# Kernel tuning notes

Measured on AMD Instinct MI355X. Metric: run time of the kernel, lower is better.

## Reference

```python
import math
import jax, jax.numpy as jnp
import numpy as np

WS = 4            # window size
LS = 2 * WS       # local context size
NH = 8            # num heads
DIM = 128
EPS = 1e-5


def setup_inputs() -> dict:
    key = jax.random.key(0)
    ks = jax.random.split(key, 8)
    B, C, H, W = 4, DIM, 48, 48
    features = jax.random.normal(ks[0], (B, C, H, W), dtype=jnp.float32)
    s = 0.02
    return {
        'features': features,
        'ln_w': jnp.ones((C,), jnp.float32),
        'ln_b': jnp.zeros((C,), jnp.float32),
        'q_w': jax.random.normal(ks[1], (C, C), jnp.float32) * s,
        'q_b': jnp.zeros((C,), jnp.float32),
        'kv_w': jax.random.normal(ks[2], (2 * C, C), jnp.float32) * s,
        'kv_b': jnp.zeros((2 * C,), jnp.float32),
        'out_w': jax.random.normal(ks[3], (C, C), jnp.float32) * s,
        'out_b': jnp.zeros((C,), jnp.float32),
    }


def _avgpool_tokens(x, k):
    # x: [B,C,H,W] -> [B, (H//k)*(W//k), C]
    B, C, H, W = x.shape
    t = x.reshape(B, C, H // k, k, W // k, k).mean(axis=(3, 5))
    return t.reshape(B, C, -1).transpose(0, 2, 1)


def reference(features, ln_w, ln_b, q_w, q_b, kv_w, kv_b, out_w, out_b):
    B, C, H, W = features.shape
    Hw, Ww = H // WS, W // WS
    nw = Hw * Ww
    hd = C // NH

    # ---- window partition: [B,C,H,W] -> [B*nw, WS*WS, C]
    qt = features.reshape(B, C, Hw, WS, Ww, WS).transpose(0, 2, 4, 3, 5, 1)
    qt = qt.reshape(B * nw, WS * WS, C)

    # ---- LayerNorm(dim)
    mu = qt.mean(-1, keepdims=True)
    var = qt.var(-1, keepdims=True)
    qt = (qt - mu) / jnp.sqrt(var + EPS) * ln_w + ln_b

    # ---- local context: pad to target, unfold kernel=LS stride=WS
    target = (int(math.sqrt(nw)) - 1) * WS + LS
    ph, pw = max(0, target - H), max(0, target - W)
    pad = ((0, 0), (0, 0), (ph // 2, ph - ph // 2), (pw // 2, pw - pw // 2))
    padded = jnp.pad(features, pad)
    # channel order of patches is (C, kh, kw), same as torch unfold
    patches = jax.lax.conv_general_dilated_patches(
        padded, filter_shape=(LS, LS), window_strides=(WS, WS), padding='VALID')
    local = patches.reshape(B, C, LS * LS, nw).transpose(0, 3, 2, 1)
    local = local.reshape(B * nw, LS * LS, C)

    # ---- multi-scale pooled tokens, broadcast to each window
    mid = _avgpool_tokens(features, 2)      # [B, M, C]
    glo = _avgpool_tokens(features, 4)      # [B, G, C]
    mid = jnp.broadcast_to(mid[:, None], (B, nw) + mid.shape[1:]).reshape(B * nw, -1, C)
    glo = jnp.broadcast_to(glo[:, None], (B, nw) + glo.shape[1:]).reshape(B * nw, -1, C)

    kv_tokens = jnp.concatenate([local, mid, glo], axis=1)  # [B*nw, Nkv, C]

    # ---- projections (torch Linear: x @ W.T + b)
    queries = qt @ q_w.T + q_b
    kv = kv_tokens @ kv_w.T + kv_b
    keys, values = kv[..., :C], kv[..., C:]

    # ---- multi-head attention
    Nq, Nkv = queries.shape[1], keys.shape[1]
    q = queries.reshape(-1, Nq, NH, hd)
    k = keys.reshape(-1, Nkv, NH, hd)
    v = values.reshape(-1, Nkv, NH, hd)
    scores = jnp.einsum('bqhd,bkhd->bhqk', q, k) / math.sqrt(hd)
    weights = jax.nn.softmax(scores, axis=-1)
    attended = jnp.einsum('bhqk,bkhd->bqhd', weights, v).reshape(-1, Nq, C)

    out = attended @ out_w.T + out_b

    # ---- window reconstruction -> [B,C,H,W]
    out = out.reshape(B, Hw, Ww, WS, WS, C).transpose(0, 5, 1, 3, 2, 4)
    out = out.reshape(B, C, H, W)
    return out + features
```

## Files before the change

### kernel.cpp

```cpp
#include <hip/hip_runtime.h>


typedef unsigned short u16;
typedef short v8s __attribute__((ext_vector_type(8)));
typedef v8s __attribute__((may_alias)) v8s_am;
typedef short v4s __attribute__((ext_vector_type(4)));
typedef v4s __attribute__((may_alias)) v4s_am;
typedef float v4f __attribute__((ext_vector_type(4)));

#define MFMA_BF16(a, b, c) __builtin_amdgcn_mfma_f32_16x16x32_bf16(a, b, c, 0, 0, 0)

#if __has_builtin(__builtin_amdgcn_mfma_f32_16x16x16bf16_1k)
#define MFMA16(a, b, c) __builtin_amdgcn_mfma_f32_16x16x16bf16_1k(a, b, c, 0, 0, 0)
#else
static __device__ __forceinline__ v4f mfma16_fb(v4s a, v4s b, v4f c) {
    v8s a8 = {a[0], a[1], a[2], a[3], 0, 0, 0, 0};
    v8s b8 = {b[0], b[1], b[2], b[3], 0, 0, 0, 0};
    return MFMA_BF16(a8, b8, c);
}
#define MFMA16(a, b, c) mfma16_fb(a, b, c)
#endif

#if __has_builtin(__builtin_amdgcn_exp2f)
#define EXP2(x) __builtin_amdgcn_exp2f(x)
#else
#define EXP2(x) exp2f(x)
#endif

__device__ __forceinline__ float b2f(u16 u) {
    union { unsigned int i; float f; } x;
    x.i = ((unsigned int)u) << 16;
    return x.f;
}
__device__ __forceinline__ u16 f2b(float f) {
    union { float f; unsigned int i; } x;
    x.f = f;
    unsigned int u = x.i;
    return (u16)((u + 0x7fffu + ((u >> 16) & 1u)) >> 16);
}

__global__ __launch_bounds__(256) void k_transpose_prep(
    const float* __restrict__ F,
    const float* __restrict__ qw, const float* __restrict__ kvw,
    const float* __restrict__ ow,
    const float* __restrict__ lnw, const float* __restrict__ lnb,
    u16* __restrict__ Xt, u16* __restrict__ Wb, float* __restrict__ MuRs)
{
    int blk = blockIdx.x;
    int t = threadIdx.x;
    if (blk >= 288) {
        int base = (blk - 288) * 4096 + t * 16;
#pragma unroll
        for (int i = 0; i < 4; ++i) {
            int idx = base + i * 4;
            const float* src; int off;
            if (idx < 16384)      { src = qw;  off = idx; }
            else if (idx < 49152) { src = kvw; off = idx - 16384; }
            else                  { src = ow;  off = idx - 49152; }
            float4 v = *(const float4*)(src + off);
            unsigned long long packed =
                (unsigned long long)f2b(v.x) |
                ((unsigned long long)f2b(v.y) << 16) |
                ((unsigned long long)f2b(v.z) << 32) |
                ((unsigned long long)f2b(v.w) << 48);
            *(unsigned long long*)(Wb + idx) = packed;
        }
        if (blk == 288) {
            Wb[65536 + t] = f2b(t < 128 ? lnw[t] : lnb[t - 128]);
        }
        return;
    }
    __shared__ u16 X[128][34];
    int b = blk / 72;
    int p0 = (blk % 72) * 32;
#pragma unroll 4
    for (int i = 0; i < 16; ++i) {
        int c = i * 8 + (t >> 5);
        int pix = t & 31;
        X[c][pix] = f2b(F[((size_t)(b * 128 + c)) * 2304 + p0 + pix]);
    }
    __syncthreads();
    int pix = t >> 3;
    int c0 = (t & 7) * 16;
    size_t row = (size_t)(b * 2304 + p0 + pix) * 128;
    float s = 0.f, s2 = 0.f;
#pragma unroll
    for (int sg = 0; sg < 2; ++sg) {
        v8s raw;
#pragma unroll
        for (int j = 0; j < 8; ++j) {
            u16 u = X[c0 + sg * 8 + j][pix];
            raw[j] = (short)u;
            float v = b2f(u);
            s += v; s2 += v * v;
        }
        *(v8s_am*)&Xt[row + c0 + sg * 8] = raw;
    }
    s += __shfl_xor(s, 1);  s2 += __shfl_xor(s2, 1);
    s += __shfl_xor(s, 2);  s2 += __shfl_xor(s2, 2);
    s += __shfl_xor(s, 4);  s2 += __shfl_xor(s2, 4);
    if ((t & 7) == 0) {
        float mean = s * (1.f / 128.f);
        float var = s2 * (1.f / 128.f) - mean * mean;
        float rstd = rsqrtf(var + 1e-5f);
        MuRs[(b * 2304 + p0 + pix) * 2]     = mean;
        MuRs[(b * 2304 + p0 + pix) * 2 + 1] = rstd;
    }
}

__global__ __launch_bounds__(256) void k_pool(
    const float* __restrict__ F, u16* __restrict__ Pml)
{
    int gid = blockIdx.x * 256 + threadIdx.x;
    int row = gid >> 4;
    int seg = gid & 15;
    v8s outv;
    if (row < 2304) {
        int b = row / 576, r = row % 576;
        int i = r / 24, j = r % 24;
#pragma unroll
        for (int jc = 0; jc < 8; ++jc) {
            int c = seg * 8 + jc;
            const float* src = F + ((size_t)(b * 128 + c)) * 2304 + (2 * i) * 48 + 2 * j;
            float2 a = *(const float2*)src;
            float2 d = *(const float2*)(src + 48);
            outv[jc] = (short)f2b((a.x + a.y + d.x + d.y) * 0.25f);
        }
    } else {
        int r2 = row - 2304;
        int b = r2 / 144, r = r2 % 144;
        int i = r / 12, j = r % 12;
#pragma unroll
        for (int jc = 0; jc < 8; ++jc) {
            int c = seg * 8 + jc;
            const float* src = F + ((size_t)(b * 128 + c)) * 2304 + (4 * i) * 48 + 4 * j;
            float s = 0.f;
#pragma unroll
            for (int di = 0; di < 4; ++di) {
                float4 v = *(const float4*)(src + di * 48);
                s += (v.x + v.y) + (v.z + v.w);
            }
            outv[jc] = (short)f2b(s * 0.0625f);
        }
    }
    *(v8s_am*)&Pml[((size_t)row) * 128 + seg * 8] = outv;
}

__global__ __launch_bounds__(256) void k_gemm_kv(
    const u16* __restrict__ Pml,
    const u16* __restrict__ W,
    const float* __restrict__ bias,
    u16* __restrict__ KVg,
    u16* __restrict__ VTg)
{
    __shared__ u16 Al[64][136];
    __shared__ u16 Wl[64][136];
    int tm = blockIdx.x * 64, tn = blockIdx.y * 64;
    int t = threadIdx.x;
    {
        int seg = t & 15, r0 = t >> 4;
#pragma unroll
        for (int i = 0; i < 4; ++i) {
            int r = r0 + 16 * i;
            *(v8s_am*)&Al[r][seg * 8] = *(const v8s_am*)&Pml[((size_t)(tm + r)) * 128 + seg * 8];
            *(v8s_am*)&Wl[r][seg * 8] = *(const v8s_am*)&W[((size_t)(tn + r)) * 128 + seg * 8];
        }
    }
    __syncthreads();
    int lane = t & 63, wave = t >> 6;
    int n15 = lane & 15, quad = lane >> 4;
    int wm = (wave & 1) * 32, wn = (wave >> 1) * 32;
    v4f acc[2][2] = {};
#pragma unroll
    for (int kc = 0; kc < 4; ++kc) {
        v8s a[2], bb[2];
#pragma unroll
        for (int im = 0; im < 2; ++im)
            a[im] = *(const v8s_am*)&Al[wm + im * 16 + n15][kc * 32 + quad * 8];
#pragma unroll
        for (int in = 0; in < 2; ++in)
            bb[in] = *(const v8s_am*)&Wl[wn + in * 16 + n15][kc * 32 + quad * 8];
#pragma unroll
        for (int im = 0; im < 2; ++im)
#pragma unroll
            for (int in = 0; in < 2; ++in)
                acc[im][in] = MFMA_BF16(a[im], bb[in], acc[im][in]);
    }
#pragma unroll
    for (int in = 0; in < 2; ++in) {
        int n = tn + wn + in * 16 + n15;
        float bv = bias[n];
#pragma unroll
        for (int im = 0; im < 2; ++im) {
            int mbase = tm + wm + im * 16 + quad * 4;
#pragma unroll
            for (int r = 0; r < 4; ++r) {
                int m = mbase + r;
                u16 h = f2b(acc[im][in][r] + bv);
                if (n < 128) {
                    KVg[((size_t)m) * 128 + n] = h;
                } else {
                    int ch = n - 128, bb2, tok;
                    if (m < 2304) { bb2 = m / 576; tok = m % 576; }
                    else { int r2 = m - 2304; bb2 = r2 / 144; tok = 576 + r2 % 144; }
                    VTg[((size_t)(bb2 * 128 + ch)) * 720 + tok] = h;
                }
            }
        }
    }
}

__global__ __launch_bounds__(256, 3) void k_attn_fused(
    const float* __restrict__ F,
    const u16* __restrict__ Xt,
    const float* __restrict__ MuRs,
    const u16* __restrict__ KVg,
    const u16* __restrict__ VTg,
    const u16* __restrict__ Wb,
    const float* __restrict__ qb,
    const float* __restrict__ kvb,
    const float* __restrict__ ob,
    float* __restrict__ Out)
{
    __shared__ u16 KB[2][64][136];
    __shared__ u16 VtAt[4][32][68];

    const u16* qwb  = Wb;
    const u16* kvwb = Wb + 16384;
    const u16* owb  = Wb + 49152;
    const u16* lnwb = Wb + 65536;
    const u16* lnbb = Wb + 65664;
    u16* At = &VtAt[0][0][0];

    int w = blockIdx.x;
    int b = w / 144, wr = (w % 144) / 12, wc = w % 12;
    int t = threadIdx.x;
    int lane = t & 63, wave = t >> 6, n15 = lane & 15, quad = lane >> 4;
    v8s zf8 = {};
    v4f zz4 = {0.f, 0.f, 0.f, 0.f};
    const float QSCALE = 0.25f * 1.44269504f;

    v8s stg[4];
#pragma unroll
    for (int i = 0; i < 4; ++i) {
        int chunk = t * 4 + i;
        stg[i] = *(const v8s_am*)&KVg[((size_t)(b * 576 + (chunk >> 4))) * 128 + (chunk & 15) * 8];
    }

    int qh = wr * 4 + (n15 >> 2), qw_ = wc * 4 + (n15 & 3);
    int qpix = b * 2304 + qh * 48 + qw_;
    float mu = MuRs[qpix * 2], rstd = MuRs[qpix * 2 + 1];
    v8s xln[4];
#pragma unroll
    for (int kc = 0; kc < 4; ++kc) {
        v8s x  = *(const v8s_am*)&Xt[(size_t)qpix * 128 + kc * 32 + quad * 8];
        v8s lw = *(const v8s_am*)&lnwb[kc * 32 + quad * 8];
        v8s lb = *(const v8s_am*)&lnbb[kc * 32 + quad * 8];
        v8s y;
#pragma unroll
        for (int j = 0; j < 8; ++j)
            y[j] = (short)f2b((b2f((u16)x[j]) - mu) * rstd * b2f((u16)lw[j]) + b2f((u16)lb[j]));
        xln[kc] = y;
    }

    v4s qf2[2];
#pragma unroll
    for (int e = 0; e < 2; ++e) {
        int n0 = wave * 16 + e * 64;
        v4f qacc = zz4;
#pragma unroll
        for (int kc = 0; kc < 4; ++kc) {
            v8s aw = *(const v8s_am*)&qwb[((size_t)(n0 + n15)) * 128 + kc * 32 + quad * 8];
            qacc = MFMA_BF16(aw, xln[kc], qacc);
        }
        v4s q4;
#pragma unroll
        for (int r = 0; r < 4; ++r)
            q4[r] = (short)f2b((qacc[r] + qb[n0 + quad * 4 + r]) * QSCALE);
        qf2[e] = q4;
    }

    v4s kfloc[2][4];
#pragma unroll
    for (int g = 0; g < 4; ++g) {
        int tl = g * 16 + n15;
        int fh = tl >> 3, fw = tl & 7;
        int hh = wr * 4 - 2 + fh, ww = wc * 4 - 2 + fw;
        bool valid = (hh >= 0 && hh < 48 && ww >= 0 && ww < 48);
        size_t arow = (size_t)(b * 2304 + hh * 48 + ww) * 128;
        v8s xb[4];
#pragma unroll
        for (int kc = 0; kc < 4; ++kc) {
            v8s v = zf8;
            if (valid) v = *(const v8s_am*)&Xt[arow + kc * 32 + quad * 8];
            xb[kc] = v;
        }
#pragma unroll
        for (int s = 0; s < 4; ++s) {
            int sbase = (s & 1) * 64 + (s >> 1) * 128 + wave * 16;
            v4f acc = zz4;
#pragma unroll
            for (int kc = 0; kc < 4; ++kc) {
                v8s aw = *(const v8s_am*)&kvwb[((size_t)(sbase + n15)) * 128 + kc * 32 + quad * 8];
                acc = MFMA_BF16(aw, xb[kc], acc);
            }
            if (s < 2) {
                v4s k4;
#pragma unroll
                for (int r = 0; r < 4; ++r)
                    k4[r] = (short)f2b(acc[r] + kvb[sbase + quad * 4 + r]);
                kfloc[s][g] = k4;
            } else {
                int e = s - 2;
#pragma unroll
                for (int r = 0; r < 4; ++r)
                    VtAt[wave][e * 16 + quad * 4 + r][g * 16 + n15] =
                        f2b(acc[r] + kvb[sbase + quad * 4 + r]);
            }
        }
    }

    v4f oacc[2] = {};
    float ls[2] = {0.f, 0.f};
    const u16* VTb = VTg + (size_t)b * 128 * 720;

    asm volatile("s_waitcnt lgkmcnt(0)" ::: "memory");
#pragma unroll
    for (int g = 0; g < 4; ++g) {
#pragma unroll
        for (int e = 0; e < 2; ++e) {
            v4f St = MFMA16(kfloc[e][g], qf2[e], zz4);
            float p0 = EXP2(St[0]), p1 = EXP2(St[1]);
            float p2 = EXP2(St[2]), p3 = EXP2(St[3]);
            ls[e] += (p0 + p1) + (p2 + p3);
            v4s pk = {(short)f2b(p0), (short)f2b(p1), (short)f2b(p2), (short)f2b(p3)};
            v4s vf = *(const v4s_am*)&VtAt[wave][e * 16 + n15][g * 16 + quad * 4];
            oacc[e] = MFMA16(vf, pk, oacc[e]);
        }
    }

#pragma unroll
    for (int i = 0; i < 4; ++i) {
        int chunk = t * 4 + i;
        *(v8s_am*)&KB[1][chunk >> 4][(chunk & 15) * 8] = stg[i];
    }
    __syncthreads();

    for (int tb = 0; tb <= 10; ++tb) {
        v4s vp[2][4];
#pragma unroll
        for (int e = 0; e < 2; ++e) {
            int head = wave + e * 4;
            const u16* vrow = VTb + (size_t)(head * 16 + n15) * 720 + tb * 64 + quad * 4;
#pragma unroll
            for (int g = 0; g < 4; ++g)
                vp[e][g] = *(const v4s_am*)(vrow + g * 16);
        }
        int nt_ = tb + 1;
        int rowbase = (nt_ < 9) ? (b * 576 + nt_ * 64)
                                : (2304 + b * 144 + nt_ * 64 - 576);
        int nrows = (nt_ == 11) ? 16 : 64;
        bool sv[4];
#pragma unroll
        for (int i = 0; i < 4; ++i) {
            int chunk = t * 4 + i;
            int rr = chunk >> 4;
            sv[i] = rr < nrows;
            if (sv[i])
                stg[i] = *(const v8s_am*)&KVg[((size_t)(rowbase + rr)) * 128 + (chunk & 15) * 8];
        }
        const u16 (*KBc)[136] = KB[1 - (tb & 1)];
#pragma unroll
        for (int g = 0; g < 4; ++g) {
#pragma unroll
            for (int e = 0; e < 2; ++e) {
                int head = wave + e * 4;
                v4s kf = *(const v4s_am*)&KBc[g * 16 + n15][head * 16 + quad * 4];
                v4f St = MFMA16(kf, qf2[e], zz4);
                float p0 = EXP2(St[0]), p1 = EXP2(St[1]);
                float p2 = EXP2(St[2]), p3 = EXP2(St[3]);
                ls[e] += (p0 + p1) + (p2 + p3);
                v4s pk = {(short)f2b(p0), (short)f2b(p1), (short)f2b(p2), (short)f2b(p3)};
                oacc[e] = MFMA16(vp[e][g], pk, oacc[e]);
            }
        }
#pragma unroll
        for (int i = 0; i < 4; ++i) {
            if (sv[i]) {
                int chunk = t * 4 + i;
                *(v8s_am*)&KB[tb & 1][chunk >> 4][(chunk & 15) * 8] = stg[i];
            }
        }
        __syncthreads();
    }
#pragma unroll
    for (int e = 0; e < 2; ++e) {
        int head = wave + e * 4;
        v4s vf = *(const v4s_am*)(VTb + (size_t)(head * 16 + n15) * 720 + 704 + quad * 4);
        v4s kf = *(const v4s_am*)&KB[0][n15][head * 16 + quad * 4];
        v4f St = MFMA16(kf, qf2[e], zz4);
        float p0 = EXP2(St[0]), p1 = EXP2(St[1]);
        float p2 = EXP2(St[2]), p3 = EXP2(St[3]);
        ls[e] += (p0 + p1) + (p2 + p3);
        v4s pk = {(short)f2b(p0), (short)f2b(p1), (short)f2b(p2), (short)f2b(p3)};
        oacc[e] = MFMA16(vf, pk, oacc[e]);
    }

#pragma unroll
    for (int e = 0; e < 2; ++e) {
        ls[e] += __shfl_xor(ls[e], 16);
        ls[e] += __shfl_xor(ls[e], 32);
        float inv = 1.f / ls[e];
        int head = wave + e * 4;
        v4s a4 = {(short)f2b(oacc[e][0] * inv), (short)f2b(oacc[e][1] * inv),
                  (short)f2b(oacc[e][2] * inv), (short)f2b(oacc[e][3] * inv)};
        *(v4s_am*)&At[n15 * 136 + head * 16 + quad * 4] = a4;
    }
    __syncthreads();

    {
        int n0 = wave * 32;
        v4f oa[2] = {};
#pragma unroll
        for (int kc = 0; kc < 4; ++kc) {
            v8s af = *(const v8s_am*)&At[n15 * 136 + kc * 32 + quad * 8];
#pragma unroll
            for (int in = 0; in < 2; ++in) {
                v8s bf = *(const v8s_am*)&owb[((size_t)(n0 + in * 16 + n15)) * 128 + kc * 32 + quad * 8];
                oa[in] = MFMA_BF16(af, bf, oa[in]);
            }
        }
#pragma unroll
        for (int in = 0; in < 2; ++in) {
            int c = n0 + in * 16 + n15;
            float bv = ob[c];
#pragma unroll
            for (int r = 0; r < 4; ++r) {
                int pix = quad * 4 + r;
                int hh = wr * 4 + (pix >> 2), ww_ = wc * 4 + (pix & 3);
                size_t idx = ((size_t)(b * 128 + c)) * 2304 + hh * 48 + ww_;
                Out[idx] = oa[in][r] + bv + F[idx];
            }
        }
    }
}

extern "C" void kernel_launch(void* const* d_in, const int* in_sizes, int n_in,
                              void* d_out, int out_size, void* d_ws, size_t ws_size,
                              hipStream_t stream)
{
    const float* F   = (const float*)d_in[0];
    const float* lnw = (const float*)d_in[1];
    const float* lnb = (const float*)d_in[2];
    const float* qw  = (const float*)d_in[3];
    const float* qb  = (const float*)d_in[4];
    const float* kvw = (const float*)d_in[5];
    const float* kvb = (const float*)d_in[6];
    const float* ow  = (const float*)d_in[7];
    const float* ob  = (const float*)d_in[8];
    float* Out = (float*)d_out;

    u16* ws    = (u16*)d_ws;
    u16* Xt    = ws;
    u16* Pml   = Xt + 9216 * 128;
    u16* KVg   = Pml + 2880 * 128;
    u16* VTg   = KVg + 2880 * 128;
    u16* Wb    = VTg + 4 * 128 * 720;
    float* MuRs = (float*)(Wb + 65792);
    u16* kvwb = Wb + 16384;

    k_transpose_prep<<<304, 256, 0, stream>>>(F, qw, kvw, ow, lnw, lnb, Xt, Wb, MuRs);
    k_pool<<<180, 256, 0, stream>>>(F, Pml);
    k_gemm_kv<<<dim3(45, 4), 256, 0, stream>>>(Pml, kvwb, kvb, KVg, VTg);
    k_attn_fused<<<576, 256, 0, stream>>>(F, Xt, MuRs, KVg, VTg, Wb,
                                          qb, kvb, ob, Out);
}
```

Before: 137.2 us.

## Load K/V fragments directly to registers with double buffering, drop LDS staging

The attention loop no longer stages the shared K tile through LDS with per-tile __syncthreads. Each wave now loads its K and V fragments straight from global memory into registers, ping-ponging between two register fragment sets so the next tile's loads overlap the current tile's MFMA and exp work. The smaller LDS footprint lets the launch bound rise to 4 blocks per CU, and block indices are remapped so each XCD handles windows of a single batch image for L2 locality. In exchange, register pressure goes up and global/L2 traffic increases, since K is no longer shared across waves through LDS.

```diff
diff --git a/kernel.cpp b/kernel.cpp
--- a/kernel.cpp
+++ b/kernel.cpp
@@ -210,7 +210,54 @@
     }
 }
 
-__global__ __launch_bounds__(256, 3) void k_attn_fused(
+struct Frag { v4s k[2][4]; v4s v[2][4]; };
+
+__device__ __forceinline__ void load_tile(Frag& f, const u16* kb0, const u16* vb0,
+                                          int rb128, int t64)
+{
+#pragma unroll
+    for (int e = 0; e < 2; ++e)
+#pragma unroll
+        for (int g = 0; g < 4; ++g) {
+            f.k[e][g] = *(const v4s_am*)(kb0 + e * 64 + rb128 + g * 2048);
+            f.v[e][g] = *(const v4s_am*)(vb0 + e * 46080 + t64 + g * 16);
+        }
+}
+
+__device__ __forceinline__ void load_tile11(Frag& f, const u16* kb0, const u16* vb0,
+                                            int b)
+{
+    int rb128 = 294912 + b * 18432 + 16384;
+#pragma unroll
+    for (int e = 0; e < 2; ++e) {
+        f.k[e][0] = *(const v4s_am*)(kb0 + e * 64 + rb128);
+        f.v[e][0] = *(const v4s_am*)(vb0 + e * 46080 + 704);
+    }
+}
+
+__device__ __forceinline__ int rb128f(int b, int t) {
+    return (t < 9) ? (b * 73728 + t * 8192) : (294912 + b * 18432 + (t - 9) * 8192);
+}
+
+template<int NG>
+__device__ __forceinline__ void tile_attn(const Frag& f, const v4s* qf2,
+                                          v4f* oacc, float* ls)
+{
+    v4f zz = {0.f, 0.f, 0.f, 0.f};
+#pragma unroll
+    for (int g = 0; g < NG; ++g)
+#pragma unroll
+        for (int e = 0; e < 2; ++e) {
+            v4f St = MFMA16(f.k[e][g], qf2[e], zz);
+            float p0 = EXP2(St[0]), p1 = EXP2(St[1]);
+            float p2 = EXP2(St[2]), p3 = EXP2(St[3]);
+            ls[e] += (p0 + p1) + (p2 + p3);
+            v4s pk = {(short)f2b(p0), (short)f2b(p1), (short)f2b(p2), (short)f2b(p3)};
+            oacc[e] = MFMA16(f.v[e][g], pk, oacc[e]);
+        }
+}
+
+__global__ __launch_bounds__(256, 4) void k_attn_fused(
     const float* __restrict__ F,
     const u16* __restrict__ Xt,
     const float* __restrict__ MuRs,
@@ -222,30 +269,26 @@
     const float* __restrict__ ob,
     float* __restrict__ Out)
 {
-    __shared__ u16 KB[2][64][136];
-    __shared__ u16 VtAt[4][32][68];
+    __shared__ u16 VtW[4][32][68];
+    __shared__ u16 At[16][136];
 
     const u16* qwb  = Wb;
     const u16* kvwb = Wb + 16384;
     const u16* owb  = Wb + 49152;
     const u16* lnwb = Wb + 65536;
     const u16* lnbb = Wb + 65664;
-    u16* At = &VtAt[0][0][0];
-
-    int w = blockIdx.x;
-    int b = w / 144, wr = (w % 144) / 12, wc = w % 12;
+
+    int blk = blockIdx.x;
+    int xcd = blk & 7, jj = blk >> 3;
+    int b = xcd >> 1;
+    int wr = (xcd & 1) * 6 + jj / 12;
+    int wc = jj % 12;
+
     int t = threadIdx.x;
     int lane = t & 63, wave = t >> 6, n15 = lane & 15, quad = lane >> 4;
     v8s zf8 = {};
     v4f zz4 = {0.f, 0.f, 0.f, 0.f};
     const float QSCALE = 0.25f * 1.44269504f;
-
-    v8s stg[4];
-#pragma unroll
-    for (int i = 0; i < 4; ++i) {
-        int chunk = t * 4 + i;
-        stg[i] = *(const v8s_am*)&KVg[((size_t)(b * 576 + (chunk >> 4))) * 128 + (chunk & 15) * 8];
-    }
 
     int qh = wr * 4 + (n15 >> 2), qw_ = wc * 4 + (n15 & 3);
     int qpix = b * 2304 + qh * 48 + qw_;
@@ -314,15 +357,19 @@
                 int e = s - 2;
 #pragma unroll
                 for (int r = 0; r < 4; ++r)
-                    VtAt[wave][e * 16 + quad * 4 + r][g * 16 + n15] =
+                    VtW[wave][e * 16 + quad * 4 + r][g * 16 + n15] =
                         f2b(acc[r] + kvb[sbase + quad * 4 + r]);
             }
         }
     }
+
+    const u16* kb0 = KVg + (size_t)n15 * 128 + wave * 16 + quad * 4;
+    const u16* vb0 = VTg + (size_t)b * 92160 + ((size_t)(wave * 16 + n15)) * 720 + quad * 4;
+    Frag fa, fb;
+    load_tile(fa, kb0, vb0, b * 73728, 0);
 
     v4f oacc[2] = {};
     float ls[2] = {0.f, 0.f};
-    const u16* VTb = VTg + (size_t)b * 128 * 720;
 
     asm volatile("s_waitcnt lgkmcnt(0)" ::: "memory");
 #pragma unroll
@@ -334,78 +381,25 @@
             float p2 = EXP2(St[2]), p3 = EXP2(St[3]);
             ls[e] += (p0 + p1) + (p2 + p3);
             v4s pk = {(short)f2b(p0), (short)f2b(p1), (short)f2b(p2), (short)f2b(p3)};
-            v4s vf = *(const v4s_am*)&VtAt[wave][e * 16 + n15][g * 16 + quad * 4];
+            v4s vf = *(const v4s_am*)&VtW[wave][e * 16 + n15][g * 16 + quad * 4];
             oacc[e] = MFMA16(vf, pk, oacc[e]);
         }
     }
 
 #pragma unroll
-    for (int i = 0; i < 4; ++i) {
-        int chunk = t * 4 + i;
-        *(v8s_am*)&KB[1][chunk >> 4][(chunk & 15) * 8] = stg[i];
-    }
-    __syncthreads();
-
-    for (int tb = 0; tb <= 10; ++tb) {
-        v4s vp[2][4];
-#pragma unroll
-        for (int e = 0; e < 2; ++e) {
-            int head = wave + e * 4;
-            const u16* vrow = VTb + (size_t)(head * 16 + n15) * 720 + tb * 64 + quad * 4;
-#pragma unroll
-            for (int g = 0; g < 4; ++g)
-                vp[e][g] = *(const v4s_am*)(vrow + g * 16);
-        }
-        int nt_ = tb + 1;
-        int rowbase = (nt_ < 9) ? (b * 576 + nt_ * 64)
-                                : (2304 + b * 144 + nt_ * 64 - 576);
-        int nrows = (nt_ == 11) ? 16 : 64;
-        bool sv[4];
-#pragma unroll
-        for (int i = 0; i < 4; ++i) {
-            int chunk = t * 4 + i;
-            int rr = chunk >> 4;
-            sv[i] = rr < nrows;
-            if (sv[i])
-                stg[i] = *(const v8s_am*)&KVg[((size_t)(rowbase + rr)) * 128 + (chunk & 15) * 8];
-        }
-        const u16 (*KBc)[136] = KB[1 - (tb & 1)];
-#pragma unroll
-        for (int g = 0; g < 4; ++g) {
-#pragma unroll
-            for (int e = 0; e < 2; ++e) {
-                int head = wave + e * 4;
-                v4s kf = *(const v4s_am*)&KBc[g * 16 + n15][head * 16 + quad * 4];
-                v4f St = MFMA16(kf, qf2[e], zz4);
-                float p0 = EXP2(St[0]), p1 = EXP2(St[1]);
-                float p2 = EXP2(St[2]), p3 = EXP2(St[3]);
-                ls[e] += (p0 + p1) + (p2 + p3);
-                v4s pk = {(short)f2b(p0), (short)f2b(p1), (short)f2b(p2), (short)f2b(p3)};
-                oacc[e] = MFMA16(vp[e][g], pk, oacc[e]);
-            }
-        }
-#pragma unroll
-        for (int i = 0; i < 4; ++i) {
-            if (sv[i]) {
-                int chunk = t * 4 + i;
-                *(v8s_am*)&KB[tb & 1][chunk >> 4][(chunk & 15) * 8] = stg[i];
-            }
-        }
-        __syncthreads();
-    }
-#pragma unroll
-    for (int e = 0; e < 2; ++e) {
-        int head = wave + e * 4;
-        v4s vf = *(const v4s_am*)(VTb + (size_t)(head * 16 + n15) * 720 + 704 + quad * 4);
-        v4s kf = *(const v4s_am*)&KB[0][n15][head * 16 + quad * 4];
-        v4f St = MFMA16(kf, qf2[e], zz4);
-        float p0 = EXP2(St[0]), p1 = EXP2(St[1]);
-        float p2 = EXP2(St[2]), p3 = EXP2(St[3]);
-        ls[e] += (p0 + p1) + (p2 + p3);
-        v4s pk = {(short)f2b(p0), (short)f2b(p1), (short)f2b(p2), (short)f2b(p3)};
-        oacc[e] = MFMA16(vf, pk, oacc[e]);
-    }
-
+    for (int tt = 0; tt <= 10; tt += 2) {
+        if (tt + 1 <= 10) load_tile(fb, kb0, vb0, rb128f(b, tt + 1), (tt + 1) * 64);
+        else              load_tile11(fb, kb0, vb0, b);
+        tile_attn<4>(fa, qf2, oacc, ls);
+        if (tt + 1 <= 10) {
+            if (tt + 2 <= 10) load_tile(fa, kb0, vb0, rb128f(b, tt + 2), (tt + 2) * 64);
+            else              load_tile11(fa, kb0, vb0, b);
+            tile_attn<4>(fb, qf2, oacc, ls);
+        }
+    }
+    tile_attn<1>(fb, qf2, oacc, ls);
+
+    u16* Atp = &At[0][0];
 #pragma unroll
     for (int e = 0; e < 2; ++e) {
         ls[e] += __shfl_xor(ls[e], 16);
@@ -414,7 +408,7 @@
         int head = wave + e * 4;
         v4s a4 = {(short)f2b(oacc[e][0] * inv), (short)f2b(oacc[e][1] * inv),
                   (short)f2b(oacc[e][2] * inv), (short)f2b(oacc[e][3] * inv)};
-        *(v4s_am*)&At[n15 * 136 + head * 16 + quad * 4] = a4;
+        *(v4s_am*)&Atp[n15 * 136 + head * 16 + quad * 4] = a4;
     }
     __syncthreads();
 
@@ -423,7 +417,7 @@
         v4f oa[2] = {};
 #pragma unroll
         for (int kc = 0; kc < 4; ++kc) {
-            v8s af = *(const v8s_am*)&At[n15 * 136 + kc * 32 + quad * 8];
+            v8s af = *(const v8s_am*)&Atp[n15 * 136 + kc * 32 + quad * 8];
 #pragma unroll
             for (int in = 0; in < 2; ++in) {
                 v8s bf = *(const v8s_am*)&owb[((size_t)(n0 + in * 16 + n15)) * 128 + kc * 32 + quad * 8];
```

After: 230.1 us. 67.7% more time.

## Merge pooling into prep kernel and give each attention head its own wave

Applied to the files above, without the earlier changes.

The pooling kernel is folded into the prep kernel as extra blocks, which removes one launch. The attention kernel moves from 256 to 512 threads, so each of the 8 waves handles a single head instead of two. This halves the per-wave register state and the serial MFMA chain, and the K tile staging is spread over twice as many threads. Block indices are also remapped so that windows from the same batch land on the same XCD, improving L2 reuse of the shared K/V. The trade-off is larger blocks, more barrier participants and possibly lower occupancy under the new launch bounds.

```diff
diff --git a/kernel.cpp b/kernel.cpp
--- a/kernel.cpp
+++ b/kernel.cpp
@@ -39,15 +39,52 @@
     return (u16)((u + 0x7fffu + ((u >> 16) & 1u)) >> 16);
 }
 
-__global__ __launch_bounds__(256) void k_transpose_prep(
+__global__ __launch_bounds__(256) void k_prep(
     const float* __restrict__ F,
     const float* __restrict__ qw, const float* __restrict__ kvw,
     const float* __restrict__ ow,
     const float* __restrict__ lnw, const float* __restrict__ lnb,
-    u16* __restrict__ Xt, u16* __restrict__ Wb, float* __restrict__ MuRs)
+    u16* __restrict__ Xt, u16* __restrict__ Wb, float* __restrict__ MuRs,
+    u16* __restrict__ Pml)
 {
     int blk = blockIdx.x;
     int t = threadIdx.x;
+    if (blk >= 304) {
+        int gid = (blk - 304) * 256 + t;
+        int row = gid >> 4;
+        int seg = gid & 15;
+        v8s outv;
+        if (row < 2304) {
+            int b = row / 576, r = row % 576;
+            int i = r / 24, j = r % 24;
+#pragma unroll
+            for (int jc = 0; jc < 8; ++jc) {
+                int c = seg * 8 + jc;
+                const float* src = F + ((size_t)(b * 128 + c)) * 2304 + (2 * i) * 48 + 2 * j;
+                float2 a = *(const float2*)src;
+                float2 d = *(const float2*)(src + 48);
+                outv[jc] = (short)f2b((a.x + a.y + d.x + d.y) * 0.25f);
+            }
+        } else {
+            int r2 = row - 2304;
+            int b = r2 / 144, r = r2 % 144;
+            int i = r / 12, j = r % 12;
+#pragma unroll
+            for (int jc = 0; jc < 8; ++jc) {
+                int c = seg * 8 + jc;
+                const float* src = F + ((size_t)(b * 128 + c)) * 2304 + (4 * i) * 48 + 4 * j;
+                float s = 0.f;
+#pragma unroll
+                for (int di = 0; di < 4; ++di) {
+                    float4 v = *(const float4*)(src + di * 48);
+                    s += (v.x + v.y) + (v.z + v.w);
+                }
+                outv[jc] = (short)f2b(s * 0.0625f);
+            }
+        }
+        *(v8s_am*)&Pml[((size_t)row) * 128 + seg * 8] = outv;
+        return;
+    }
     if (blk >= 288) {
         int base = (blk - 288) * 4096 + t * 16;
 #pragma unroll
@@ -108,44 +145,6 @@
     }
 }
 
-__global__ __launch_bounds__(256) void k_pool(
-    const float* __restrict__ F, u16* __restrict__ Pml)
-{
-    int gid = blockIdx.x * 256 + threadIdx.x;
-    int row = gid >> 4;
-    int seg = gid & 15;
-    v8s outv;
-    if (row < 2304) {
-        int b = row / 576, r = row % 576;
-        int i = r / 24, j = r % 24;
-#pragma unroll
-        for (int jc = 0; jc < 8; ++jc) {
-            int c = seg * 8 + jc;
-            const float* src = F + ((size_t)(b * 128 + c)) * 2304 + (2 * i) * 48 + 2 * j;
-            float2 a = *(const float2*)src;
-            float2 d = *(const float2*)(src + 48);
-            outv[jc] = (short)f2b((a.x + a.y + d.x + d.y) * 0.25f);
-        }
-    } else {
-        int r2 = row - 2304;
-        int b = r2 / 144, r = r2 % 144;
-        int i = r / 12, j = r % 12;
-#pragma unroll
-        for (int jc = 0; jc < 8; ++jc) {
-            int c = seg * 8 + jc;
-            const float* src = F + ((size_t)(b * 128 + c)) * 2304 + (4 * i) * 48 + 4 * j;
-            float s = 0.f;
-#pragma unroll
-            for (int di = 0; di < 4; ++di) {
-                float4 v = *(const float4*)(src + di * 48);
-                s += (v.x + v.y) + (v.z + v.w);
-            }
-            outv[jc] = (short)f2b(s * 0.0625f);
-        }
-    }
-    *(v8s_am*)&Pml[((size_t)row) * 128 + seg * 8] = outv;
-}
-
 __global__ __launch_bounds__(256) void k_gemm_kv(
     const u16* __restrict__ Pml,
     const u16* __restrict__ W,
@@ -210,7 +209,7 @@
     }
 }
 
-__global__ __launch_bounds__(256, 3) void k_attn_fused(
+__global__ __launch_bounds__(512, 4) void k_attn_fused(
     const float* __restrict__ F,
     const u16* __restrict__ Xt,
     const float* __restrict__ MuRs,
@@ -223,30 +222,27 @@
     float* __restrict__ Out)
 {
     __shared__ u16 KB[2][64][136];
-    __shared__ u16 VtAt[4][32][68];
+    __shared__ u16 VtW[8][16][68];
 
     const u16* qwb  = Wb;
     const u16* kvwb = Wb + 16384;
     const u16* owb  = Wb + 49152;
     const u16* lnwb = Wb + 65536;
     const u16* lnbb = Wb + 65664;
-    u16* At = &VtAt[0][0][0];
-
-    int w = blockIdx.x;
-    int b = w / 144, wr = (w % 144) / 12, wc = w % 12;
+    u16* Atp = &VtW[0][0][0];
+
+    int blk = blockIdx.x;
+    int xcd = blk & 7, jj = blk >> 3;
+    int b = xcd >> 1;
+    int wr = (xcd & 1) * 6 + jj / 12;
+    int wc = jj % 12;
+
     int t = threadIdx.x;
     int lane = t & 63, wave = t >> 6, n15 = lane & 15, quad = lane >> 4;
     v8s zf8 = {};
     v4f zz4 = {0.f, 0.f, 0.f, 0.f};
     const float QSCALE = 0.25f * 1.44269504f;
 
-    v8s stg[4];
-#pragma unroll
-    for (int i = 0; i < 4; ++i) {
-        int chunk = t * 4 + i;
-        stg[i] = *(const v8s_am*)&KVg[((size_t)(b * 576 + (chunk >> 4))) * 128 + (chunk & 15) * 8];
-    }
-
     int qh = wr * 4 + (n15 >> 2), qw_ = wc * 4 + (n15 & 3);
     int qpix = b * 2304 + qh * 48 + qw_;
     float mu = MuRs[qpix * 2], rstd = MuRs[qpix * 2 + 1];
@@ -263,24 +259,21 @@
         xln[kc] = y;
     }
 
-    v4s qf2[2];
-#pragma unroll
-    for (int e = 0; e < 2; ++e) {
-        int n0 = wave * 16 + e * 64;
+    v4s qf;
+    {
+        int n0 = wave * 16;
         v4f qacc = zz4;
 #pragma unroll
         for (int kc = 0; kc < 4; ++kc) {
             v8s aw = *(const v8s_am*)&qwb[((size_t)(n0 + n15)) * 128 + kc * 32 + quad * 8];
             qacc = MFMA_BF16(aw, xln[kc], qacc);
         }
-        v4s q4;
 #pragma unroll
         for (int r = 0; r < 4; ++r)
-            q4[r] = (short)f2b((qacc[r] + qb[n0 + quad * 4 + r]) * QSCALE);
-        qf2[e] = q4;
-    }
-
-    v4s kfloc[2][4];
+            qf[r] = (short)f2b((qacc[r] + qb[n0 + quad * 4 + r]) * QSCALE);
+    }
+
+    v4s kfloc[4];
 #pragma unroll
     for (int g = 0; g < 4; ++g) {
         int tl = g * 16 + n15;
@@ -296,74 +289,75 @@
             xb[kc] = v;
         }
 #pragma unroll
-        for (int s = 0; s < 4; ++s) {
-            int sbase = (s & 1) * 64 + (s >> 1) * 128 + wave * 16;
+        for (int s = 0; s < 2; ++s) {
+            int sbase = s * 128 + wave * 16;
             v4f acc = zz4;
 #pragma unroll
             for (int kc = 0; kc < 4; ++kc) {
                 v8s aw = *(const v8s_am*)&kvwb[((size_t)(sbase + n15)) * 128 + kc * 32 + quad * 8];
                 acc = MFMA_BF16(aw, xb[kc], acc);
             }
-            if (s < 2) {
+            if (s == 0) {
                 v4s k4;
 #pragma unroll
                 for (int r = 0; r < 4; ++r)
                     k4[r] = (short)f2b(acc[r] + kvb[sbase + quad * 4 + r]);
-                kfloc[s][g] = k4;
+                kfloc[g] = k4;
             } else {
-                int e = s - 2;
 #pragma unroll
                 for (int r = 0; r < 4; ++r)
-                    VtAt[wave][e * 16 + quad * 4 + r][g * 16 + n15] =
+                    VtW[wave][quad * 4 + r][g * 16 + n15] =
                         f2b(acc[r] + kvb[sbase + quad * 4 + r]);
             }
         }
     }
 
-    v4f oacc[2] = {};
-    float ls[2] = {0.f, 0.f};
-    const u16* VTb = VTg + (size_t)b * 128 * 720;
+    v8s stg[2];
+#pragma unroll
+    for (int i = 0; i < 2; ++i) {
+        int chunk = i * 512 + t;
+        stg[i] = *(const v8s_am*)&KVg[((size_t)(b * 576 + (chunk >> 4))) * 128 + (chunk & 15) * 8];
+    }
+
+    v4f oacc = zz4;
+    float ls = 0.f;
+    const u16* VTb = VTg + (size_t)b * 92160;
 
     asm volatile("s_waitcnt lgkmcnt(0)" ::: "memory");
 #pragma unroll
     for (int g = 0; g < 4; ++g) {
-#pragma unroll
-        for (int e = 0; e < 2; ++e) {
-            v4f St = MFMA16(kfloc[e][g], qf2[e], zz4);
-            float p0 = EXP2(St[0]), p1 = EXP2(St[1]);
-            float p2 = EXP2(St[2]), p3 = EXP2(St[3]);
-            ls[e] += (p0 + p1) + (p2 + p3);
-            v4s pk = {(short)f2b(p0), (short)f2b(p1), (short)f2b(p2), (short)f2b(p3)};
-            v4s vf = *(const v4s_am*)&VtAt[wave][e * 16 + n15][g * 16 + quad * 4];
-            oacc[e] = MFMA16(vf, pk, oacc[e]);
-        }
-    }
-
-#pragma unroll
-    for (int i = 0; i < 4; ++i) {
-        int chunk = t * 4 + i;
+        v4f St = MFMA16(kfloc[g], qf, zz4);
+        float p0 = EXP2(St[0]), p1 = EXP2(St[1]);
+        float p2 = EXP2(St[2]), p3 = EXP2(St[3]);
+        ls += (p0 + p1) + (p2 + p3);
+        v4s pk = {(short)f2b(p0), (short)f2b(p1), (short)f2b(p2), (short)f2b(p3)};
+        v4s vf = *(const v4s_am*)&VtW[wave][n15][g * 16 + quad * 4];
+        oacc = MFMA16(vf, pk, oacc);
+    }
+
+#pragma unroll
+    for (int i = 0; i < 2; ++i) {
+        int chunk = i * 512 + t;
         *(v8s_am*)&KB[1][chunk >> 4][(chunk & 15) * 8] = stg[i];
     }
     __syncthreads();
 
     for (int tb = 0; tb <= 10; ++tb) {
-        v4s vp[2][4];
-#pragma unroll
-        for (int e = 0; e < 2; ++e) {
-            int head = wave + e * 4;
-            const u16* vrow = VTb + (size_t)(head * 16 + n15) * 720 + tb * 64 + quad * 4;
+        v4s vp[4];
+        {
+            const u16* vrow = VTb + (size_t)(wave * 16 + n15) * 720 + tb * 64 + quad * 4;
 #pragma unroll
             for (int g = 0; g < 4; ++g)
-                vp[e][g] = *(const v4s_am*)(vrow + g * 16);
+                vp[g] = *(const v4s_am*)(vrow + g * 16);
         }
         int nt_ = tb + 1;
         int rowbase = (nt_ < 9) ? (b * 576 + nt_ * 64)
                                 : (2304 + b * 144 + nt_ * 64 - 576);
         int nrows = (nt_ == 11) ? 16 : 64;
-        bool sv[4];
-#pragma unroll
-        for (int i = 0; i < 4; ++i) {
-            int chunk = t * 4 + i;
+        bool sv[2];
+#pragma unroll
+        for (int i = 0; i < 2; ++i) {
+            int chunk = i * 512 + t;
             int rr = chunk >> 4;
             sv[i] = rr < nrows;
             if (sv[i])
@@ -372,75 +366,61 @@
         const u16 (*KBc)[136] = KB[1 - (tb & 1)];
 #pragma unroll
         for (int g = 0; g < 4; ++g) {
-#pragma unroll
-            for (int e = 0; e < 2; ++e) {
-                int head = wave + e * 4;
-                v4s kf = *(const v4s_am*)&KBc[g * 16 + n15][head * 16 + quad * 4];
-                v4f St = MFMA16(kf, qf2[e], zz4);
-                float p0 = EXP2(St[0]), p1 = EXP2(St[1]);
-                float p2 = EXP2(St[2]), p3 = EXP2(St[3]);
-                ls[e] += (p0 + p1) + (p2 + p3);
-                v4s pk = {(short)f2b(p0), (short)f2b(p1), (short)f2b(p2), (short)f2b(p3)};
-                oacc[e] = MFMA16(vp[e][g], pk, oacc[e]);
-            }
-        }
-#pragma unroll
-        for (int i = 0; i < 4; ++i) {
+            v4s kf = *(const v4s_am*)&KBc[g * 16 + n15][wave * 16 + quad * 4];
+            v4f St = MFMA16(kf, qf, zz4);
+            float p0 = EXP2(St[0]), p1 = EXP2(St[1]);
+            float p2 = EXP2(St[2]), p3 = EXP2(St[3]);
+            ls += (p0 + p1) + (p2 + p3);
+            v4s pk = {(short)f2b(p0), (short)f2b(p1), (short)f2b(p2), (short)f2b(p3)};
+            oacc = MFMA16(vp[g], pk, oacc);
+        }
+#pragma unroll
+        for (int i = 0; i < 2; ++i) {
             if (sv[i]) {
-                int chunk = t * 4 + i;
+                int chunk = i * 512 + t;
                 *(v8s_am*)&KB[tb & 1][chunk >> 4][(chunk & 15) * 8] = stg[i];
             }
         }
         __syncthreads();
     }
-#pragma unroll
-    for (int e = 0; e < 2; ++e) {
-        int head = wave + e * 4;
-        v4s vf = *(const v4s_am*)(VTb + (size_t)(head * 16 + n15) * 720 + 704 + quad * 4);
-        v4s kf = *(const v4s_am*)&KB[0][n15][head * 16 + quad * 4];
-        v4f St = MFMA16(kf, qf2[e], zz4);
+    {
+        v4s vf = *(const v4s_am*)(VTb + (size_t)(wave * 16 + n15) * 720 + 704 + quad * 4);
+        v4s kf = *(const v4s_am*)&KB[0][n15][wave * 16 + quad * 4];
+        v4f St = MFMA16(kf, qf, zz4);
         float p0 = EXP2(St[0]), p1 = EXP2(St[1]);
         float p2 = EXP2(St[2]), p3 = EXP2(St[3]);
-        ls[e] += (p0 + p1) + (p2 + p3);
+        ls += (p0 + p1) + (p2 + p3);
         v4s pk = {(short)f2b(p0), (short)f2b(p1), (short)f2b(p2), (short)f2b(p3)};
-        oacc[e] = MFMA16(vf, pk, oacc[e]);
-    }
-
-#pragma unroll
-    for (int e = 0; e < 2; ++e) {
-        ls[e] += __shfl_xor(ls[e], 16);
-        ls[e] += __shfl_xor(ls[e], 32);
-        float inv = 1.f / ls[e];
-        int head = wave + e * 4;
-        v4s a4 = {(short)f2b(oacc[e][0] * inv), (short)f2b(oacc[e][1] * inv),
-                  (short)f2b(oacc[e][2] * inv), (short)f2b(oacc[e][3] * inv)};
-        *(v4s_am*)&At[n15 * 136 + head * 16 + quad * 4] = a4;
+        oacc = MFMA16(vf, pk, oacc);
+    }
+
+    ls += __shfl_xor(ls, 16);
+    ls += __shfl_xor(ls, 32);
+    {
+        float inv = 1.f / ls;
+        v4s a4 = {(short)f2b(oacc[0] * inv), (short)f2b(oacc[1] * inv),
+                  (short)f2b(oacc[2] * inv), (short)f2b(oacc[3] * inv)};
+        *(v4s_am*)&Atp[n15 * 136 + wave * 16 + quad * 4] = a4;
     }
     __syncthreads();
 
     {
-        int n0 = wave * 32;
-        v4f oa[2] = {};
+        int n0 = wave * 16;
+        v4f oa = zz4;
 #pragma unroll
         for (int kc = 0; kc < 4; ++kc) {
-            v8s af = *(const v8s_am*)&At[n15 * 136 + kc * 32 + quad * 8];
-#pragma unroll
-            for (int in = 0; in < 2; ++in) {
-                v8s bf = *(const v8s_am*)&owb[((size_t)(n0 + in * 16 + n15)) * 128 + kc * 32 + quad * 8];
-                oa[in] = MFMA_BF16(af, bf, oa[in]);
-            }
-        }
-#pragma unroll
-        for (int in = 0; in < 2; ++in) {
-            int c = n0 + in * 16 + n15;
-            float bv = ob[c];
-#pragma unroll
-            for (int r = 0; r < 4; ++r) {
-                int pix = quad * 4 + r;
-                int hh = wr * 4 + (pix >> 2), ww_ = wc * 4 + (pix & 3);
-                size_t idx = ((size_t)(b * 128 + c)) * 2304 + hh * 48 + ww_;
-                Out[idx] = oa[in][r] + bv + F[idx];
-            }
+            v8s af = *(const v8s_am*)&Atp[n15 * 136 + kc * 32 + quad * 8];
+            v8s bf = *(const v8s_am*)&owb[((size_t)(n0 + n15)) * 128 + kc * 32 + quad * 8];
+            oa = MFMA_BF16(af, bf, oa);
+        }
+        int c = n0 + n15;
+        float bv = ob[c];
+#pragma unroll
+        for (int r = 0; r < 4; ++r) {
+            int pix = quad * 4 + r;
+            int hh = wr * 4 + (pix >> 2), ww_ = wc * 4 + (pix & 3);
+            size_t idx = ((size_t)(b * 128 + c)) * 2304 + hh * 48 + ww_;
+            Out[idx] = oa[r] + bv + F[idx];
         }
     }
 }
@@ -469,9 +449,8 @@
     float* MuRs = (float*)(Wb + 65792);
     u16* kvwb = Wb + 16384;
 
-    k_transpose_prep<<<304, 256, 0, stream>>>(F, qw, kvw, ow, lnw, lnb, Xt, Wb, MuRs);
-    k_pool<<<180, 256, 0, stream>>>(F, Pml);
+    k_prep<<<484, 256, 0, stream>>>(F, qw, kvw, ow, lnw, lnb, Xt, Wb, MuRs, Pml);
     k_gemm_kv<<<dim3(45, 4), 256, 0, stream>>>(Pml, kvwb, kvb, KVg, VTg);
-    k_attn_fused<<<576, 256, 0, stream>>>(F, Xt, MuRs, KVg, VTg, Wb,
+    k_attn_fused<<<576, 512, 0, stream>>>(F, Xt, MuRs, KVg, VTg, Wb,
                                           qb, kvb, ob, Out);
 }
```

Result: no change. 135.1 us (-1.5%).
